# Optimization experiments

Hardware: AMD Instinct MI355X
Metric: run time of the kernel (lower is better)

Reference implementation:

```python
import jax, jax.numpy as jnp
import numpy as np

B, H, W = 4, 512, 512
NOI = 4
LMBDA = 1.0
RHO = 1.0
ALPHA = 1.8
MU = 1.0
C = RHO / (MU + RHO)

QTAB = np.array([16,11,10,16,24,40,51,61,
                 12,12,14,19,26,58,60,55,
                 14,13,16,24,40,57,69,56,
                 14,17,22,29,51,87,80,62,
                 18,22,37,56,68,109,103,77,
                 24,35,55,64,81,104,113,92,
                 49,64,78,87,103,121,120,101,
                 72,92,95,98,112,100,103,99], dtype=np.float32) / 255.0

def _dct_basis():
    xs = 2.0 * np.arange(8) + 1.0
    us = np.pi * np.arange(8) / 16.0
    a = np.ones(8, np.float64); a[0] = 1.0 / np.sqrt(2.0)
    cos = np.cos(np.outer(xs, us)) * a[None, :]          # [x, u]
    F = 0.25 * np.einsum('xu,yv->xyuv', cos, cos).reshape(8, 8, 64)
    return jnp.asarray(F, jnp.float32)

F_DCT = _dct_basis()                                     # [8,8,64]
Q = jnp.asarray(QTAB).reshape(1, 1, 1, 64)

# tf.image kernels (rows index input channel)
K_RGB2YUV = jnp.array([[0.299, -0.14714119, 0.61497538],
                       [0.587, -0.28886916, -0.51496512],
                       [0.114,  0.43601035, -0.10001026]], jnp.float32)
K_YUV2RGB = jnp.array([[1.0, 1.0, 1.0],
                       [0.0, -0.394642334, 2.03206185],
                       [1.13988303, -0.58062185, 0.0]], jnp.float32)

def _dct_blocks(x):
    # x: [B,h*8,w*8] single channel -> [B,h,w,64]; equals stride-8 conv with DCT filters
    b, hh, ww = x.shape
    blk = x.reshape(b, hh // 8, 8, ww // 8, 8)
    return jnp.einsum('bhiwj,ijk->bhwk', blk, F_DCT)

def _idct_blocks(c):
    # c: [B,h,w,64] -> [B,h*8,w*8]; equals depth_to_space + IDCT conv + depth_to_space
    b, hh, ww, _ = c.shape
    img = jnp.einsum('bhwk,ijk->bhiwj', c, F_DCT)
    return img.reshape(b, hh * 8, ww * 8)

def _W(rgb):
    # RGB2JPEG_Coef: rgb -> (y_coefs, u_coefs, v_coefs)
    yuv = rgb @ K_RGB2YUV
    y = yuv[..., 0] - 0.5
    u, v = yuv[..., 1], yuv[..., 2]
    def ds(t):  # 2x2 average pool
        b, hh, ww = t.shape
        return t.reshape(b, hh // 2, 2, ww // 2, 2).mean(axis=(2, 4))
    return (_dct_blocks(y), _dct_blocks(ds(u)), _dct_blocks(ds(v)))

def _Wt(coefs):
    # JPEG_Coef2RGB: (y_c, u_c, v_c) -> rgb
    yc, uc, vc = coefs
    y = jnp.clip(_idct_blocks(yc) + 0.5, 0.0, 1.0)
    def up(t):
        return jnp.repeat(jnp.repeat(t, 2, axis=1), 2, axis=2)
    u = jnp.clip(up(_idct_blocks(uc)), -0.5, 0.5)
    v = jnp.clip(up(_idct_blocks(vc)), -0.5, 0.5)
    yuv = jnp.stack([y, u, v], axis=-1)
    return jnp.clip(yuv @ K_YUV2RGB, 0.0, 1.0)

def _quant_adjust(Wx, r):
    # QuantizationAdjustment: piecewise-best of 3 candidates, elementwise
    y = Wx + C * r
    ry = Q * jnp.round(y / Q)
    sgn_r = jnp.sign(r)
    hqm = Q / 2 - 1.0 / 510.0
    hqp = Q / 2 + 1.0 / 510.0
    def err(d):
        return (MU / 2) * jnp.square(C * r + d) + \
               (RHO / 2) * jnp.square(-MU / (MU + RHO) + Q * jnp.round((y + d) / Q) - y)
    c1 = -sgn_r * jnp.minimum(C * jnp.abs(r), jnp.abs(ry - y - sgn_r * Q * hqm))
    c2 = ry - hqp * Q * jnp.sign(y - ry - C * r) - y
    c3 = -sgn_r * jnp.minimum(C * jnp.abs(r), jnp.abs(ry - y - sgn_r * Q * (1.0 + hqm)))
    best = jnp.where(err(c2) < err(c1), c2, c1)
    return jnp.where(err(c3) < err(best), c3, best)

def _forward(img):
    hh, ww = img.shape[1], img.shape[2]
    # XUpdate: FFT-domain proxy solve with filters [0,1] (vertical / horizontal)
    k1 = jnp.zeros((hh, ww), jnp.float32).at[1, 0].set(1.0)
    k2 = jnp.zeros((hh, ww), jnp.float32).at[0, 1].set(1.0)
    F1 = jnp.fft.rfft2(k1)
    F2 = jnp.fft.rfft2(k2)
    A = 1.0 + LMBDA * (jnp.abs(F1) ** 2 + jnp.abs(F2) ** 2)  # [H, W//2+1]
    def xup(t):
        Tf = jnp.fft.rfft2(t, axes=(1, 2))
        return jnp.fft.irfft2(Tf / A[None, :, :, None], s=(hh, ww), axes=(1, 2))

    Ws = _W(img)
    negC = tuple(Q * jnp.round(w / Q) for w in Ws)
    y = img
    By = negC
    u = tuple(jnp.zeros_like(w) for w in Ws)

    for _ in range(NOI):
        x = xup(y)
        AxplusC = tuple((1.0 - ALPHA) * By[c] - (2.0 - ALPHA) * negC[c] for c in range(3))
        Wx = _W(x)
        r = tuple(-AxplusC[c] - Wx[c] - u[c] for c in range(3))
        Wdz = tuple(_quant_adjust(Wx[c], r[c]) for c in range(3))
        y = x + C * _Wt(r) + _Wt(Wdz)
        By = tuple(Q * jnp.round((Wx[c] + C * r[c] + Wdz[c]) / Q) for c in range(3))
        u = tuple(u[c] + AxplusC[c] + By[c] for c in range(3))

    return xup(y)

def setup_inputs() -> dict:
    key = jax.random.key(0)
    s = jax.random.uniform(key, (B, H, W, 3), dtype=jnp.float32)
    return {"s": s}

def reference(s) -> jnp.ndarray:
    return _forward(s)
```

## Files before the change

kernel.cpp:

```cpp
#include <hip/hip_runtime.h>
#include <math.h>

#define H1 0.49039264020161522f
#define H2 0.46193976625564338f
#define H3 0.41573480615127262f
#define H4 0.35355339059327376f
#define H5 0.27778511650980111f
#define H6 0.19134171618254489f
#define H7 0.09754516100806413f

__device__ __constant__ float cBB[64] = {
  H4,  H1,  H2,  H3,  H4,  H5,  H6,  H7,
  H4,  H3,  H6, -H7, -H4, -H1, -H2, -H5,
  H4,  H5, -H6, -H1, -H4,  H7,  H2,  H3,
  H4,  H7, -H2, -H5,  H4,  H3, -H6, -H1,
  H4, -H7, -H2,  H5,  H4, -H3, -H6,  H1,
  H4, -H5, -H6,  H1, -H4, -H7,  H2, -H3,
  H4, -H3,  H6,  H7, -H4,  H1, -H2,  H5,
  H4, -H1,  H2, -H3,  H4, -H5,  H6, -H7,
};

__device__ __constant__ float cQ[64] = {
  16.f/255.f, 11.f/255.f, 10.f/255.f, 16.f/255.f, 24.f/255.f, 40.f/255.f, 51.f/255.f, 61.f/255.f,
  12.f/255.f, 12.f/255.f, 14.f/255.f, 19.f/255.f, 26.f/255.f, 58.f/255.f, 60.f/255.f, 55.f/255.f,
  14.f/255.f, 13.f/255.f, 16.f/255.f, 24.f/255.f, 40.f/255.f, 57.f/255.f, 69.f/255.f, 56.f/255.f,
  14.f/255.f, 17.f/255.f, 22.f/255.f, 29.f/255.f, 51.f/255.f, 87.f/255.f, 80.f/255.f, 62.f/255.f,
  18.f/255.f, 22.f/255.f, 37.f/255.f, 56.f/255.f, 68.f/255.f, 109.f/255.f, 103.f/255.f, 77.f/255.f,
  24.f/255.f, 35.f/255.f, 55.f/255.f, 64.f/255.f, 81.f/255.f, 104.f/255.f, 113.f/255.f, 92.f/255.f,
  49.f/255.f, 64.f/255.f, 78.f/255.f, 87.f/255.f, 103.f/255.f, 121.f/255.f, 120.f/255.f, 101.f/255.f,
  72.f/255.f, 92.f/255.f, 95.f/255.f, 98.f/255.f, 112.f/255.f, 100.f/255.f, 103.f/255.f, 99.f/255.f,
};

__device__ __forceinline__ float clampf(float x, float lo, float hi) {
    return fminf(fmaxf(x, lo), hi);
}
__device__ __forceinline__ float sgnf(float x) {
    return (x > 0.f) ? 1.f : ((x < 0.f) ? -1.f : 0.f);
}

__global__ __launch_bounds__(256)
void smooth_jpeg_kernel(const float* __restrict__ s, float* __restrict__ out)
{
    const int t    = threadIdx.x;
    const int py   = t >> 4, px = t & 15;
    const int tile = blockIdx.x;
    const int b    = tile >> 10;
    const int ti   = tile & 1023;
    const int gy   = (ti >> 5) * 16 + py;
    const int gx   = (ti & 31) * 16 + px;

    __shared__ float BBl[64];
    __shared__ float Ql[64];
    __shared__ float ly[256];
    __shared__ float tmpa[256];
    __shared__ float tmpb[256];
    __shared__ float tmpc[256];
    __shared__ float lu[64];
    __shared__ float lv[64];
    __shared__ float cR[384];
    __shared__ float cWz[384];

    if (t < 64) { BBl[t] = cBB[t]; Ql[t] = cQ[t]; }

    const size_t pixbase = (((size_t)b * 512 + gy) * 512 + gx) * 3;
    const float sr = s[pixbase + 0];
    const float sg = s[pixbase + 1];
    const float sb = s[pixbase + 2];

    const int kY   = t & 63;
    const int blkY = t >> 6;
    const int byB  = blkY >> 1, bxB = blkY & 1;

    float negY = 0.f, byY = 0.f, uY = 0.f;
    float negC2 = 0.f, byC2 = 0.f, uC2 = 0.f;

    auto phaseA = [&](float pr, float pg, float pb) {
        __syncthreads();
        float yv = 0.299f*pr + 0.587f*pg + 0.114f*pb - 0.5f;
        float uu = -0.14714119f*pr - 0.28886916f*pg + 0.43601035f*pb;
        float vv =  0.61497538f*pr - 0.51496512f*pg - 0.10001026f*pb;
        ly[t] = yv;
        float ub = __shfl_xor(uu, 1),  uc = __shfl_xor(uu, 16), ud = __shfl_xor(uu, 17);
        float vb = __shfl_xor(vv, 1),  vc = __shfl_xor(vv, 16), vd = __shfl_xor(vv, 17);
        if ((t & 17) == 0) {
            int ci = ((py >> 1) << 3) + (px >> 1);
            lu[ci] = 0.25f * (((uu + ub) + uc) + ud);
            lv[ci] = 0.25f * (((vv + vb) + vc) + vd);
        }
    };

    auto phaseC = [&]() {
        __syncthreads();
        int v = t & 7;
        float bv[8];
        #pragma unroll
        for (int j = 0; j < 8; ++j) bv[j] = BBl[j*8 + v];
        {
            int rowi = t >> 4, bx = (t >> 3) & 1;
            const float* src = &ly[rowi*16 + bx*8];
            float acc = 0.f;
            #pragma unroll
            for (int j = 0; j < 8; ++j) acc = fmaf(src[j], bv[j], acc);
            tmpa[t] = acc;
        }
        if (t < 128) {
            int p = t >> 6, r8 = (t >> 3) & 7;
            const float* src = (p ? lv : lu) + r8*8;
            float acc = 0.f;
            #pragma unroll
            for (int j = 0; j < 8; ++j) acc = fmaf(src[j], bv[j], acc);
            tmpb[t] = acc;
        }
    };

    auto colDCT = [&](float& wy, float& wc) {
        __syncthreads();
        int u = kY >> 3, v = kY & 7;
        float bu[8];
        #pragma unroll
        for (int i = 0; i < 8; ++i) bu[i] = BBl[i*8 + u];
        float acc = 0.f;
        #pragma unroll
        for (int i = 0; i < 8; ++i)
            acc = fmaf(tmpa[(byB*8 + i)*16 + bxB*8 + v], bu[i], acc);
        wy = acc;
        if (t < 128) {
            float accc = 0.f;
            #pragma unroll
            for (int i = 0; i < 8; ++i)
                accc = fmaf(tmpb[(t & 64) + i*8 + v], bu[i], accc);
            wc = accc;
        }
    };

    auto quant = [&](float wx, float neg, float& by, float& uu, int idx) {
        float q    = Ql[idx & 63];
        float axc  = -0.8f*by - 0.2f*neg;
        float r    = -axc - wx - uu;
        float yq   = wx + 0.5f*r;
        float r0   = rintf(yq / q);
        float ry   = q * r0;
        float sgn  = sgnf(r);
        float hqm  = 0.5f*q - (1.0f/510.0f);
        float hqp  = 0.5f*q + (1.0f/510.0f);
        float aa   = 0.5f*fabsf(r);
        float b1   = fabsf(ry - yq - sgn*q*hqm);
        float b3   = fabsf(ry - yq - sgn*q*(1.0f + hqm));
        float c1   = -sgn * fminf(aa, b1);
        float c3   = -sgn * fminf(aa, b3);
        float sarg = yq - ry - 0.5f*r;
        float sg2  = sgnf(sarg);
        float c2   = ry - hqp*q*sg2 - yq;
        float rint1 = rintf((yq + c1) / q);
        float rint3 = rintf((yq + c3) / q);
        float rint2 = r0;
        float a1 = 0.5f*r + c1;
        float a2 = 0.5f*r + c2;
        float a3 = 0.5f*r + c3;
        float e1 = (-0.5f + q*rint1) - yq;
        float e2 = (-0.5f + q*rint2) - yq;
        float e3 = (-0.5f + q*rint3) - yq;
        float err1 = 0.5f*a1*a1 + 0.5f*e1*e1;
        float err2 = 0.5f*a2*a2 + 0.5f*e2*e2;
        float err3 = 0.5f*a3*a3 + 0.5f*e3*e3;
        bool p2 = err2 < err1;
        float best = p2 ? c2 : c1;
        float ebst = p2 ? err2 : err1;
        float rbst = p2 ? rint2 : rint1;
        bool p3 = err3 < ebst;
        float wdz  = p3 ? c3 : best;
        float rwin = p3 ? rint3 : rbst;
        cR[idx]  = r;
        cWz[idx] = wdz;
        by = q * rwin;
        uu = (uu + axc) + by;
    };

    auto phaseE = [&]() {
        __syncthreads();
        int u = kY >> 3, j = kY & 7;
        float bj[8];
        #pragma unroll
        for (int v = 0; v < 8; ++v) bj[v] = BBl[j*8 + v];
        const float* csrc = ((blkY < 2) ? cR : cWz) + 256 + (blkY & 1)*64 + u*8;
        float acc = 0.f;
        #pragma unroll
        for (int v = 0; v < 8; ++v) acc = fmaf(csrc[v], bj[v], acc);
        ly[t] = acc;
        const float* r_src = cR  + blkY*64 + u*8;
        const float* w_src = cWz + blkY*64 + u*8;
        float aR = 0.f, aW = 0.f;
        #pragma unroll
        for (int v = 0; v < 8; ++v) {
            aR = fmaf(r_src[v], bj[v], aR);
            aW = fmaf(w_src[v], bj[v], aW);
        }
        tmpc[t] = aR;
        tmpb[t] = aW;
    };

    auto phaseF = [&]() {
        __syncthreads();
        int i = kY >> 3, j = kY & 7;
        float bi[8];
        #pragma unroll
        for (int u = 0; u < 8; ++u) bi[u] = BBl[i*8 + u];
        float acc = 0.f;
        #pragma unroll
        for (int u = 0; u < 8; ++u) acc = fmaf(ly[blkY*64 + u*8 + j], bi[u], acc);
        tmpa[t] = acc;
    };

    phaseA(sr, sg, sb);
    phaseC();
    {
        float wy = 0.f, wc = 0.f;
        colDCT(wy, wc);
        float q = Ql[kY];
        negY = q * rintf(wy / q); byY = negY; uY = 0.f;
        if (t < 128) { negC2 = q * rintf(wc / q); byC2 = negC2; uC2 = 0.f; }
    }

    float yr = sr, yg = sg, yb = sb;

    #pragma unroll 1
    for (int it = 0; it < 4; ++it) {
        const float xr = yr * (1.0f/3.0f);
        const float xg = yg * (1.0f/3.0f);
        const float xb = yb * (1.0f/3.0f);

        phaseA(xr, xg, xb);
        phaseC();
        float wy = 0.f, wc = 0.f;
        colDCT(wy, wc);
        quant(wy, negY, byY, uY, t);
        if (t < 128) quant(wc, negC2, byC2, uC2, 256 + t);
        phaseE();
        phaseF();

        __syncthreads();
        {
            int blk = ((py >> 3) << 1) + (px >> 3);
            int i = py & 7, j = px & 7;
            float bi[8];
            #pragma unroll
            for (int u = 0; u < 8; ++u) bi[u] = BBl[i*8 + u];
            float accR = 0.f, accW = 0.f;
            #pragma unroll
            for (int u = 0; u < 8; ++u) {
                accR = fmaf(tmpc[blk*64 + u*8 + j], bi[u], accR);
                accW = fmaf(tmpb[blk*64 + u*8 + j], bi[u], accW);
            }
            int kuv = ((py >> 1) << 3) + (px >> 1);
            float uR = clampf(tmpa[kuv],       -0.5f, 0.5f);
            float vR = clampf(tmpa[64 + kuv],  -0.5f, 0.5f);
            float uW = clampf(tmpa[128 + kuv], -0.5f, 0.5f);
            float vW = clampf(tmpa[192 + kuv], -0.5f, 0.5f);
            float yR = clampf(accR + 0.5f, 0.f, 1.f);
            float yW = clampf(accW + 0.5f, 0.f, 1.f);
            float rR = clampf(yR + 1.13988303f*vR, 0.f, 1.f);
            float gR = clampf(yR - 0.394642334f*uR - 0.58062185f*vR, 0.f, 1.f);
            float bR = clampf(yR + 2.03206185f*uR, 0.f, 1.f);
            float rW = clampf(yW + 1.13988303f*vW, 0.f, 1.f);
            float gW = clampf(yW - 0.394642334f*uW - 0.58062185f*vW, 0.f, 1.f);
            float bW = clampf(yW + 2.03206185f*uW, 0.f, 1.f);
            yr = xr + 0.5f*rR + rW;
            yg = xg + 0.5f*gR + gW;
            yb = xb + 0.5f*bR + bW;
        }
    }

    out[pixbase + 0] = yr * (1.0f/3.0f);
    out[pixbase + 1] = yg * (1.0f/3.0f);
    out[pixbase + 2] = yb * (1.0f/3.0f);
}

extern "C" void kernel_launch(void* const* d_in, const int* in_sizes, int n_in,
                              void* d_out, int out_size, void* d_ws, size_t ws_size,
                              hipStream_t stream) {
    const float* s = (const float*)d_in[0];
    float* out = (float*)d_out;
    smooth_jpeg_kernel<<<dim3(4096), dim3(256), 0, stream>>>(s, out);
}
```

Baseline: 49.13 us.

## Map each wavefront to one 8x8 block and do DCTs via ds_bpermute

The thread-to-pixel mapping changes so that each 64-lane wavefront owns one 8x8 luma block. The separable forward and inverse DCTs then exchange data across lanes with ds_bpermute instead of staging every pass through shared memory. This removes several shared-memory round trips and __syncthreads barriers per iteration, and quantization constants are hoisted into registers. In exchange it adds many bpermute operations, which still go through the LDS hardware. The chroma paths still use shared memory, so the remaining barriers are kept.

```diff
diff --git a/kernel.cpp b/kernel.cpp
--- a/kernel.cpp
+++ b/kernel.cpp
@@ -37,120 +37,138 @@
 __device__ __forceinline__ float sgnf(float x) {
     return (x > 0.f) ? 1.f : ((x < 0.f) ? -1.f : 0.f);
 }
+__device__ __forceinline__ float bperm(int byteIdx, float v) {
+    return __int_as_float(__builtin_amdgcn_ds_bpermute(byteIdx, __float_as_int(v)));
+}
 
 __global__ __launch_bounds__(256)
 void smooth_jpeg_kernel(const float* __restrict__ s, float* __restrict__ out)
 {
-    const int t    = threadIdx.x;
-    const int py   = t >> 4, px = t & 15;
+    const int t  = threadIdx.x;
+    const int l  = t & 63;
+    const int w  = t >> 6;
+    const int li = l >> 3, lj = l & 7;
+    const int by = w >> 1, bx = w & 1;
+
     const int tile = blockIdx.x;
-    const int b    = tile >> 10;
-    const int ti   = tile & 1023;
-    const int gy   = (ti >> 5) * 16 + py;
-    const int gx   = (ti & 31) * 16 + px;
-
-    __shared__ float BBl[64];
-    __shared__ float Ql[64];
-    __shared__ float ly[256];
-    __shared__ float tmpa[256];
-    __shared__ float tmpb[256];
-    __shared__ float tmpc[256];
-    __shared__ float lu[64];
-    __shared__ float lv[64];
-    __shared__ float cR[384];
-    __shared__ float cWz[384];
-
-    if (t < 64) { BBl[t] = cBB[t]; Ql[t] = cQ[t]; }
+    const int b  = tile >> 10;
+    const int ti = tile & 1023;
+    const int gy = (ti >> 5) * 16 + by * 8 + li;
+    const int gx = (ti & 31) * 16 + bx * 8 + lj;
+
+    __shared__ __align__(16) float BBr[64];
+    __shared__ __align__(16) float BBt[64];
+    __shared__ __align__(16) float lu[64];
+    __shared__ __align__(16) float lv[64];
+    __shared__ __align__(16) float crc[128];
+    __shared__ __align__(16) float cwzc[128];
+    __shared__ __align__(16) float tmpch[256];
+
+    if (t < 64) { BBr[t] = cBB[t]; BBt[t] = cBB[(t & 7) * 8 + (t >> 3)]; }
 
     const size_t pixbase = (((size_t)b * 512 + gy) * 512 + gx) * 3;
     const float sr = s[pixbase + 0];
     const float sg = s[pixbase + 1];
     const float sb = s[pixbase + 2];
 
-    const int kY   = t & 63;
-    const int blkY = t >> 6;
-    const int byB  = blkY >> 1, bxB = blkY & 1;
-
-    float negY = 0.f, byY = 0.f, uY = 0.f;
-    float negC2 = 0.f, byC2 = 0.f, uC2 = 0.f;
-
-    auto phaseA = [&](float pr, float pg, float pb) {
-        __syncthreads();
+    const float q     = cQ[l];
+    const float hqm   = 0.5f*q - (1.0f/510.0f);
+    const float qhqm1 = q * hqm;
+    const float qhqm3 = q * (1.0f + hqm);
+    const float qhqp  = (0.5f*q + (1.0f/510.0f)) * q;
+
+    const int addrA   = (l & 56) * 4;
+    const int addrB   = (l & 7) * 4;
+    const int rowOffA = (l & 7) * 8;
+    const int rowOffB = (l >> 3) * 8;
+
+    auto load8 = [](const float* p, float* d) {
+        float4 a = *reinterpret_cast<const float4*>(p);
+        float4 c = *reinterpret_cast<const float4*>(p + 4);
+        d[0]=a.x; d[1]=a.y; d[2]=a.z; d[3]=a.w;
+        d[4]=c.x; d[5]=c.y; d[6]=c.z; d[7]=c.w;
+    };
+
+    auto fwd2d = [&](float val) -> float {
+        float cA[8]; load8(&BBt[rowOffA], cA);
+        float rs = 0.f;
+        #pragma unroll
+        for (int jj = 0; jj < 8; ++jj) rs = fmaf(bperm(addrA + 4*jj, val), cA[jj], rs);
+        float cB[8]; load8(&BBt[rowOffB], cB);
+        float acc = 0.f;
+        #pragma unroll
+        for (int ii = 0; ii < 8; ++ii) acc = fmaf(bperm(addrB + 32*ii, rs), cB[ii], acc);
+        return acc;
+    };
+
+    auto fwd2d_lds = [&](const float* plane) -> float {
+        float cA[8]; load8(&BBt[rowOffA], cA);
+        const float* rowp = plane + (l >> 3) * 8;
+        float rs = 0.f;
+        #pragma unroll
+        for (int jj = 0; jj < 8; ++jj) rs = fmaf(rowp[jj], cA[jj], rs);
+        float cB[8]; load8(&BBt[rowOffB], cB);
+        float acc = 0.f;
+        #pragma unroll
+        for (int ii = 0; ii < 8; ++ii) acc = fmaf(bperm(addrB + 32*ii, rs), cB[ii], acc);
+        return acc;
+    };
+
+    auto inv2d = [&](float coef) -> float {
+        float rA[8]; load8(&BBr[rowOffA], rA);
+        float s1 = 0.f;
+        #pragma unroll
+        for (int v = 0; v < 8; ++v) s1 = fmaf(bperm(addrA + 4*v, coef), rA[v], s1);
+        float rB[8]; load8(&BBr[rowOffB], rB);
+        float acc = 0.f;
+        #pragma unroll
+        for (int u = 0; u < 8; ++u) acc = fmaf(bperm(addrB + 32*u, s1), rB[u], acc);
+        return acc;
+    };
+
+    auto inv2d_lds = [&](const float* coefs) -> float {
+        float rA[8]; load8(&BBr[rowOffA], rA);
+        const float* rowp = coefs + (l >> 3) * 8;
+        float s1 = 0.f;
+        #pragma unroll
+        for (int v = 0; v < 8; ++v) s1 = fmaf(rowp[v], rA[v], s1);
+        float rB[8]; load8(&BBr[rowOffB], rB);
+        float acc = 0.f;
+        #pragma unroll
+        for (int u = 0; u < 8; ++u) acc = fmaf(bperm(addrB + 32*u, s1), rB[u], acc);
+        return acc;
+    };
+
+    auto phaseA = [&](float pr, float pg, float pb) -> float {
         float yv = 0.299f*pr + 0.587f*pg + 0.114f*pb - 0.5f;
         float uu = -0.14714119f*pr - 0.28886916f*pg + 0.43601035f*pb;
         float vv =  0.61497538f*pr - 0.51496512f*pg - 0.10001026f*pb;
-        ly[t] = yv;
-        float ub = __shfl_xor(uu, 1),  uc = __shfl_xor(uu, 16), ud = __shfl_xor(uu, 17);
-        float vb = __shfl_xor(vv, 1),  vc = __shfl_xor(vv, 16), vd = __shfl_xor(vv, 17);
-        if ((t & 17) == 0) {
-            int ci = ((py >> 1) << 3) + (px >> 1);
-            lu[ci] = 0.25f * (((uu + ub) + uc) + ud);
-            lv[ci] = 0.25f * (((vv + vb) + vc) + vd);
-        }
-    };
-
-    auto phaseC = [&]() {
-        __syncthreads();
-        int v = t & 7;
-        float bv[8];
-        #pragma unroll
-        for (int j = 0; j < 8; ++j) bv[j] = BBl[j*8 + v];
-        {
-            int rowi = t >> 4, bx = (t >> 3) & 1;
-            const float* src = &ly[rowi*16 + bx*8];
-            float acc = 0.f;
-            #pragma unroll
-            for (int j = 0; j < 8; ++j) acc = fmaf(src[j], bv[j], acc);
-            tmpa[t] = acc;
-        }
-        if (t < 128) {
-            int p = t >> 6, r8 = (t >> 3) & 7;
-            const float* src = (p ? lv : lu) + r8*8;
-            float acc = 0.f;
-            #pragma unroll
-            for (int j = 0; j < 8; ++j) acc = fmaf(src[j], bv[j], acc);
-            tmpb[t] = acc;
-        }
-    };
-
-    auto colDCT = [&](float& wy, float& wc) {
-        __syncthreads();
-        int u = kY >> 3, v = kY & 7;
-        float bu[8];
-        #pragma unroll
-        for (int i = 0; i < 8; ++i) bu[i] = BBl[i*8 + u];
-        float acc = 0.f;
-        #pragma unroll
-        for (int i = 0; i < 8; ++i)
-            acc = fmaf(tmpa[(byB*8 + i)*16 + bxB*8 + v], bu[i], acc);
-        wy = acc;
-        if (t < 128) {
-            float accc = 0.f;
-            #pragma unroll
-            for (int i = 0; i < 8; ++i)
-                accc = fmaf(tmpb[(t & 64) + i*8 + v], bu[i], accc);
-            wc = accc;
-        }
-    };
-
-    auto quant = [&](float wx, float neg, float& by, float& uu, int idx) {
-        float q    = Ql[idx & 63];
-        float axc  = -0.8f*by - 0.2f*neg;
-        float r    = -axc - wx - uu;
-        float yq   = wx + 0.5f*r;
-        float r0   = rintf(yq / q);
-        float ry   = q * r0;
-        float sgn  = sgnf(r);
-        float hqm  = 0.5f*q - (1.0f/510.0f);
-        float hqp  = 0.5f*q + (1.0f/510.0f);
-        float aa   = 0.5f*fabsf(r);
-        float b1   = fabsf(ry - yq - sgn*q*hqm);
-        float b3   = fabsf(ry - yq - sgn*q*(1.0f + hqm));
-        float c1   = -sgn * fminf(aa, b1);
-        float c3   = -sgn * fminf(aa, b3);
+        float ub = __shfl_xor(uu, 1), uc = __shfl_xor(uu, 8), ud = __shfl_xor(uu, 9);
+        float vb = __shfl_xor(vv, 1), vc = __shfl_xor(vv, 8), vd = __shfl_xor(vv, 9);
+        if ((l & 9) == 0) {
+            int ci = by*4 + (li >> 1), cj = bx*4 + (lj >> 1);
+            lu[ci*8 + cj] = 0.25f * (((uu + ub) + uc) + ud);
+            lv[ci*8 + cj] = 0.25f * (((vv + vb) + vc) + vd);
+        }
+        return yv;
+    };
+
+    auto quant = [&](float wx, float neg, float& byS, float& uuS,
+                     float& r_out, float& wz_out) {
+        float axc = -0.8f*byS - 0.2f*neg;
+        float r   = -axc - wx - uuS;
+        float yq  = wx + 0.5f*r;
+        float r0  = rintf(yq / q);
+        float ry  = q * r0;
+        float sgn = sgnf(r);
+        float aa  = 0.5f*fabsf(r);
+        float b1  = fabsf(ry - yq - sgn*qhqm1);
+        float b3  = fabsf(ry - yq - sgn*qhqm3);
+        float c1  = -sgn * fminf(aa, b1);
+        float c3  = -sgn * fminf(aa, b3);
         float sarg = yq - ry - 0.5f*r;
         float sg2  = sgnf(sarg);
-        float c2   = ry - hqp*q*sg2 - yq;
+        float c2   = ry - qhqp*sg2 - yq;
         float rint1 = rintf((yq + c1) / q);
         float rint3 = rintf((yq + c3) / q);
         float rint2 = r0;
@@ -170,56 +188,25 @@
         bool p3 = err3 < ebst;
         float wdz  = p3 ? c3 : best;
         float rwin = p3 ? rint3 : rbst;
-        cR[idx]  = r;
-        cWz[idx] = wdz;
-        by = q * rwin;
-        uu = (uu + axc) + by;
-    };
-
-    auto phaseE = [&]() {
-        __syncthreads();
-        int u = kY >> 3, j = kY & 7;
-        float bj[8];
-        #pragma unroll
-        for (int v = 0; v < 8; ++v) bj[v] = BBl[j*8 + v];
-        const float* csrc = ((blkY < 2) ? cR : cWz) + 256 + (blkY & 1)*64 + u*8;
-        float acc = 0.f;
-        #pragma unroll
-        for (int v = 0; v < 8; ++v) acc = fmaf(csrc[v], bj[v], acc);
-        ly[t] = acc;
-        const float* r_src = cR  + blkY*64 + u*8;
-        const float* w_src = cWz + blkY*64 + u*8;
-        float aR = 0.f, aW = 0.f;
-        #pragma unroll
-        for (int v = 0; v < 8; ++v) {
-            aR = fmaf(r_src[v], bj[v], aR);
-            aW = fmaf(w_src[v], bj[v], aW);
-        }
-        tmpc[t] = aR;
-        tmpb[t] = aW;
-    };
-
-    auto phaseF = [&]() {
-        __syncthreads();
-        int i = kY >> 3, j = kY & 7;
-        float bi[8];
-        #pragma unroll
-        for (int u = 0; u < 8; ++u) bi[u] = BBl[i*8 + u];
-        float acc = 0.f;
-        #pragma unroll
-        for (int u = 0; u < 8; ++u) acc = fmaf(ly[blkY*64 + u*8 + j], bi[u], acc);
-        tmpa[t] = acc;
-    };
-
-    phaseA(sr, sg, sb);
-    phaseC();
+        r_out  = r;
+        wz_out = wdz;
+        byS = q * rwin;
+        uuS = (uuS + axc) + byS;
+    };
+
+    float pixY = phaseA(sr, sg, sb);
+    __syncthreads();
+    float negY, byY, uY = 0.f;
+    float negC = 0.f, byC = 0.f, uC = 0.f;
     {
-        float wy = 0.f, wc = 0.f;
-        colDCT(wy, wc);
-        float q = Ql[kY];
-        negY = q * rintf(wy / q); byY = negY; uY = 0.f;
-        if (t < 128) { negC2 = q * rintf(wc / q); byC2 = negC2; uC2 = 0.f; }
+        float wy = fwd2d(pixY);
+        negY = q * rintf(wy / q); byY = negY;
+        if (w < 2) {
+            float wc = fwd2d_lds(w ? lv : lu);
+            negC = q * rintf(wc / q); byC = negC;
+        }
     }
+    __syncthreads();
 
     float yr = sr, yg = sg, yb = sb;
 
@@ -229,33 +216,40 @@
         const float xg = yg * (1.0f/3.0f);
         const float xb = yb * (1.0f/3.0f);
 
-        phaseA(xr, xg, xb);
-        phaseC();
-        float wy = 0.f, wc = 0.f;
-        colDCT(wy, wc);
-        quant(wy, negY, byY, uY, t);
-        if (t < 128) quant(wc, negC2, byC2, uC2, 256 + t);
-        phaseE();
-        phaseF();
-
+        float pY = phaseA(xr, xg, xb);
         __syncthreads();
+
+        float wy = fwd2d(pY);
+        float rY, wzY;
+        quant(wy, negY, byY, uY, rY, wzY);
+
+        if (w < 2) {
+            float wc = fwd2d_lds(w ? lv : lu);
+            float rC, wzC;
+            quant(wc, negC, byC, uC, rC, wzC);
+            crc[w*64 + l]  = rC;
+            cwzc[w*64 + l] = wzC;
+        }
+
+        float accR = inv2d(rY);
+        float accW = inv2d(wzY);
+        __syncthreads();
+
         {
-            int blk = ((py >> 3) << 1) + (px >> 3);
-            int i = py & 7, j = px & 7;
-            float bi[8];
-            #pragma unroll
-            for (int u = 0; u < 8; ++u) bi[u] = BBl[i*8 + u];
-            float accR = 0.f, accW = 0.f;
-            #pragma unroll
-            for (int u = 0; u < 8; ++u) {
-                accR = fmaf(tmpc[blk*64 + u*8 + j], bi[u], accR);
-                accW = fmaf(tmpb[blk*64 + u*8 + j], bi[u], accW);
-            }
-            int kuv = ((py >> 1) << 3) + (px >> 1);
-            float uR = clampf(tmpa[kuv],       -0.5f, 0.5f);
-            float vR = clampf(tmpa[64 + kuv],  -0.5f, 0.5f);
-            float uW = clampf(tmpa[128 + kuv], -0.5f, 0.5f);
-            float vW = clampf(tmpa[192 + kuv], -0.5f, 0.5f);
+            const float* csrc = (w == 0) ? crc
+                              : (w == 1) ? crc + 64
+                              : (w == 2) ? cwzc
+                              :            cwzc + 64;
+            tmpch[w*64 + l] = inv2d_lds(csrc);
+        }
+        __syncthreads();
+
+        {
+            int kuv = (by*4 + (li >> 1))*8 + (bx*4 + (lj >> 1));
+            float uR = clampf(tmpch[kuv],        -0.5f, 0.5f);
+            float vR = clampf(tmpch[64 + kuv],   -0.5f, 0.5f);
+            float uW = clampf(tmpch[128 + kuv],  -0.5f, 0.5f);
+            float vW = clampf(tmpch[192 + kuv],  -0.5f, 0.5f);
             float yR = clampf(accR + 0.5f, 0.f, 1.f);
             float yW = clampf(accW + 0.5f, 0.f, 1.f);
             float rR = clampf(yR + 1.13988303f*vR, 0.f, 1.f);
```

Result: slower. 67.51 us (+37.4%).
